# Optimization experiments

Hardware: AMD Instinct MI355X
Metric: run time of the kernel (lower is better)

## Reference

```python
import jax, jax.numpy as jnp
import numpy as np

B, T, N, F = 32, 4096, 11, 16
NUM_LABS = 20
H = 2 * F  # refine hidden dim
LN_EPS = 1e-5


def setup_inputs() -> dict:
    key = jax.random.key(0)
    ks = jax.random.split(key, 8)
    x = jax.random.normal(ks[0], (B, T, N, F), dtype=jnp.float32)
    lab_idx = jax.random.randint(ks[1], (B,), 0, NUM_LABS)
    # projection: identity + small noise, per lab
    projection = (jnp.eye(N, dtype=jnp.float32)[None].repeat(NUM_LABS, axis=0)
                  + 0.01 * jax.random.normal(ks[2], (NUM_LABS, N, N), dtype=jnp.float32))
    bias = jnp.zeros((NUM_LABS, 1, N, F), dtype=jnp.float32)
    w1 = jax.random.normal(ks[3], (F, H), dtype=jnp.float32) / np.sqrt(F)
    b1 = jnp.zeros((H,), dtype=jnp.float32)
    ln_g = jnp.ones((H,), dtype=jnp.float32)
    ln_b = jnp.zeros((H,), dtype=jnp.float32)
    w2 = jax.random.normal(ks[4], (H, F), dtype=jnp.float32) / np.sqrt(H)
    b2 = jnp.zeros((F,), dtype=jnp.float32)
    return {"x": x, "lab_idx": lab_idx, "projection": projection, "bias": bias,
            "w1": w1, "b1": b1, "ln_g": ln_g, "ln_b": ln_b, "w2": w2, "b2": b2}


def reference(x, lab_idx, projection, bias, w1, b1, ln_g, ln_b, w2, b2):
    # gather per-sample projection / bias by lab index
    W = projection[lab_idx]          # [b, n, n]
    Bb = bias[lab_idx]               # [b, 1, n, f]
    # torch: bmm(x^T, W) then transpose -> out[b,t,m,f] = sum_n x[b,t,n,f] * W[b,n,m]
    out = jnp.einsum('btnf,bnm->btmf', x, W) + Bb
    # refine MLP: Linear -> LayerNorm -> GELU(exact) -> Linear
    h = out @ w1 + b1                                    # [b,t,n,2f]
    mu = jnp.mean(h, axis=-1, keepdims=True)
    var = jnp.var(h, axis=-1, keepdims=True)
    h = (h - mu) / jnp.sqrt(var + LN_EPS) * ln_g + ln_b
    h = jax.nn.gelu(h, approximate=False)
    return h @ w2 + b2
```

## Files before the change

kernel.cpp:

```cpp
#include <hip/hip_runtime.h>
#include <hip/hip_bf16.h>
#include <math.h>

#define BB 32
#define TT 4096
#define NN 11
#define FF 16
#define HH 32
#define LN_EPS 1e-5f
#define TOTAL_ROWS (BB * TT * NN)
#define ROWS_PER_BLOCK 256
#define NBLOCKS (TOTAL_ROWS / ROWS_PER_BLOCK)
#define BLOCKS_PER_BATCH (TT * NN / ROWS_PER_BLOCK)

typedef __attribute__((ext_vector_type(8))) short short8;
typedef __attribute__((ext_vector_type(4))) float f32x4;

union Frag { unsigned u[4]; uint4 u4; short8 v; };

__device__ __forceinline__ unsigned pack2_bf16(float a, float b) {
    __hip_bfloat162 p = __float22bfloat162_rn(make_float2(a, b));
    union { __hip_bfloat162 h; unsigned u; } cvt; cvt.h = p; return cvt.u;
}
__device__ __forceinline__ unsigned short to_bf16u(float a) {
    __hip_bfloat16 h = __float2bfloat16(a);
    union { __hip_bfloat16 h; unsigned short u; } cvt; cvt.h = h; return cvt.u;
}

__device__ __forceinline__ float fast_gelu(float v) {
    const float v2 = v * v;
    const float c  = fmaf(0.044715f, v2, 1.0f);
    const float t  = v * c * 1.5957691216057308f;
    const float e  = __expf(-t);
    return v * __builtin_amdgcn_rcpf(1.0f + e);
}

__global__ __launch_bounds__(256) void fused_proj_mlp_mfma(
    const float* __restrict__ x,
    const int*   __restrict__ lab_idx,
    const float* __restrict__ proj,
    const float* __restrict__ bias,
    const float* __restrict__ w1,
    const float* __restrict__ b1,
    const float* __restrict__ ln_g,
    const float* __restrict__ ln_b,
    const float* __restrict__ w2,
    const float* __restrict__ b2,
    float*       __restrict__ out)
{
    __shared__ unsigned o_st[4][64][12];
    __shared__ unsigned short h_st[4][4][16][40];

    const int tid  = threadIdx.x;
    const int wv   = tid >> 6;
    const int lane = tid & 63;
    const int q    = lane >> 4;
    const int c    = lane & 15;

    const int row      = blockIdx.x * ROWS_PER_BLOCK + tid;
    const unsigned token = (unsigned)row / 11u;
    const int m        = row - (int)(token * 11u);
    const int bidx     = blockIdx.x / BLOCKS_PER_BATCH;
    const int lab      = lab_idx[bidx];

    Frag b1a, b1b, b2f;
    #pragma unroll
    for (int d = 0; d < 4; ++d) {
        const int k0 = 8 * q + 2 * d;
        float wa0 = 0.f, wa1 = 0.f, wb0 = 0.f, wb1 = 0.f;
        if (q < 2) {
            wa0 = w1[k0 * HH + c];        wa1 = w1[(k0 + 1) * HH + c];
            wb0 = w1[k0 * HH + 16 + c];   wb1 = w1[(k0 + 1) * HH + 16 + c];
        }
        b1a.u[d] = pack2_bf16(wa0, wa1);
        b1b.u[d] = pack2_bf16(wb0, wb1);
        b2f.u[d] = pack2_bf16(w2[k0 * FF + c], w2[(k0 + 1) * FF + c]);
    }
    const float b1c_a = b1[c], b1c_b = b1[16 + c], b2c = b2[c];

    float g8[8], e8[8];
    {
        const float4* gp = reinterpret_cast<const float4*>(ln_g + 8 * q);
        const float4* bp = reinterpret_cast<const float4*>(ln_b + 8 * q);
        float4 g0 = gp[0], g1 = gp[1], e0 = bp[0], e1 = bp[1];
        g8[0]=g0.x; g8[1]=g0.y; g8[2]=g0.z; g8[3]=g0.w;
        g8[4]=g1.x; g8[5]=g1.y; g8[6]=g1.z; g8[7]=g1.w;
        e8[0]=e0.x; e8[1]=e0.y; e8[2]=e0.z; e8[3]=e0.w;
        e8[4]=e1.x; e8[5]=e1.y; e8[6]=e1.z; e8[7]=e1.w;
    }

    const float4* xp4 = reinterpret_cast<const float4*>(x) + (size_t)token * (NN * FF / 4);
    const float*  Wp  = proj + (size_t)lab * (NN * NN) + m;
    const float4* bp4 = reinterpret_cast<const float4*>(bias) + (size_t)lab * (NN * FF / 4) + m * (FF / 4);

    float o[FF];
    #pragma unroll
    for (int f4 = 0; f4 < FF / 4; ++f4) {
        float4 v = bp4[f4];
        o[f4*4+0] = v.x; o[f4*4+1] = v.y; o[f4*4+2] = v.z; o[f4*4+3] = v.w;
    }
    #pragma unroll
    for (int n = 0; n < NN; ++n) {
        const float wnm = Wp[n * NN];
        #pragma unroll
        for (int f4 = 0; f4 < FF / 4; ++f4) {
            float4 v = xp4[n * (FF / 4) + f4];
            o[f4*4+0] = fmaf(v.x, wnm, o[f4*4+0]);
            o[f4*4+1] = fmaf(v.y, wnm, o[f4*4+1]);
            o[f4*4+2] = fmaf(v.z, wnm, o[f4*4+2]);
            o[f4*4+3] = fmaf(v.w, wnm, o[f4*4+3]);
        }
    }

    {
        unsigned op[8];
        #pragma unroll
        for (int d = 0; d < 8; ++d) op[d] = pack2_bf16(o[2*d], o[2*d+1]);
        uint4* dst = reinterpret_cast<uint4*>(&o_st[wv][lane][0]);
        dst[0] = make_uint4(op[0], op[1], op[2], op[3]);
        dst[1] = make_uint4(op[4], op[5], op[6], op[7]);
    }
    __syncthreads();

    const int qo = (q & 1) * 4;

    #pragma unroll
    for (int tt = 0; tt < 4; ++tt) {
        Frag a1;
        a1.u4 = *reinterpret_cast<const uint4*>(&o_st[wv][tt * 16 + c][qo]);
        f32x4 acc1a = { b1c_a, b1c_a, b1c_a, b1c_a };
        f32x4 acc1b = { b1c_b, b1c_b, b1c_b, b1c_b };
        acc1a = __builtin_amdgcn_mfma_f32_16x16x32_bf16(a1.v, b1a.v, acc1a, 0, 0, 0);
        acc1b = __builtin_amdgcn_mfma_f32_16x16x32_bf16(a1.v, b1b.v, acc1b, 0, 0, 0);

        #pragma unroll
        for (int i = 0; i < 4; ++i) {
            h_st[wv][tt][q * 4 + i][c]      = to_bf16u(acc1a[i]);
            h_st[wv][tt][q * 4 + i][16 + c] = to_bf16u(acc1b[i]);
        }
        __syncthreads();

        Frag a2r;
        a2r.u4 = *reinterpret_cast<const uint4*>(&h_st[wv][tt][c][8 * q]);
        float hv[8];
        #pragma unroll
        for (int d = 0; d < 4; ++d) {
            union { unsigned u; float f; } lo, hi;
            lo.u = a2r.u[d] << 16; hi.u = a2r.u[d] & 0xffff0000u;
            hv[2*d] = lo.f; hv[2*d+1] = hi.f;
        }

        float s = 0.f, ss = 0.f;
        #pragma unroll
        for (int d = 0; d < 8; ++d) { s += hv[d]; ss = fmaf(hv[d], hv[d], ss); }
        s  += __shfl_xor(s, 16);  s  += __shfl_xor(s, 32);
        ss += __shfl_xor(ss, 16); ss += __shfl_xor(ss, 32);
        const float mu   = s * (1.f / HH);
        const float var  = ss * (1.f / HH) - mu * mu;
        const float rstd = rsqrtf(var + LN_EPS);
        const float nb   = -mu * rstd;

        Frag a2;
        #pragma unroll
        for (int d = 0; d < 4; ++d) {
            float v0 = fmaf(fmaf(hv[2*d],   rstd, nb), g8[2*d],   e8[2*d]);
            float v1 = fmaf(fmaf(hv[2*d+1], rstd, nb), g8[2*d+1], e8[2*d+1]);
            a2.u[d] = pack2_bf16(fast_gelu(v0), fast_gelu(v1));
        }

        f32x4 acc2 = { b2c, b2c, b2c, b2c };
        acc2 = __builtin_amdgcn_mfma_f32_16x16x32_bf16(a2.v, b2f.v, acc2, 0, 0, 0);

        float* orow = out + ((size_t)(blockIdx.x * ROWS_PER_BLOCK + wv * 64 + tt * 16 + q * 4) * FF + c);
        #pragma unroll
        for (int i = 0; i < 4; ++i) orow[(size_t)i * FF] = acc2[i];
    }
}

extern "C" void kernel_launch(void* const* d_in, const int* in_sizes, int n_in,
                              void* d_out, int out_size, void* d_ws, size_t ws_size,
                              hipStream_t stream) {
    const float* x       = (const float*)d_in[0];
    const int*   lab_idx = (const int*)  d_in[1];
    const float* proj    = (const float*)d_in[2];
    const float* bias    = (const float*)d_in[3];
    const float* w1      = (const float*)d_in[4];
    const float* b1      = (const float*)d_in[5];
    const float* ln_g    = (const float*)d_in[6];
    const float* ln_b    = (const float*)d_in[7];
    const float* w2      = (const float*)d_in[8];
    const float* b2      = (const float*)d_in[9];
    float* out = (float*)d_out;

    fused_proj_mlp_mfma<<<NBLOCKS, 256, 0, stream>>>(
        x, lab_idx, proj, bias, w1, b1, ln_g, ln_b, w2, b2, out);
}
```

Before: 222.9 us.

## Transpose MFMA operands to keep hidden activations in registers

Swaps the MFMA operand roles so the weights become the A operand and the projected activations the B operand. Each lane then holds full hidden columns in its accumulators, so LayerNorm and GELU run directly on the fp32 MFMA results. This removes the bf16 round trip through the shared-memory h_st buffer and the block-wide __syncthreads inside the loop, and drops the barrier after the o_st write. The second matmul's input is rearranged with cross-lane shuffles instead, and outputs are written as float4 stores. The cost is extra shuffle instructions, and correctness now relies on each wave reading only its own o_st region without a barrier.

```diff
diff --git a/kernel.cpp b/kernel.cpp
--- a/kernel.cpp
+++ b/kernel.cpp
@@ -22,10 +22,6 @@
     __hip_bfloat162 p = __float22bfloat162_rn(make_float2(a, b));
     union { __hip_bfloat162 h; unsigned u; } cvt; cvt.h = p; return cvt.u;
 }
-__device__ __forceinline__ unsigned short to_bf16u(float a) {
-    __hip_bfloat16 h = __float2bfloat16(a);
-    union { __hip_bfloat16 h; unsigned short u; } cvt; cvt.h = h; return cvt.u;
-}
 
 __device__ __forceinline__ float fast_gelu(float v) {
     const float v2 = v * v;
@@ -35,7 +31,7 @@
     return v * __builtin_amdgcn_rcpf(1.0f + e);
 }
 
-__global__ __launch_bounds__(256) void fused_proj_mlp_mfma(
+__global__ __launch_bounds__(256) void fused_proj_mlp_t(
     const float* __restrict__ x,
     const int*   __restrict__ lab_idx,
     const float* __restrict__ proj,
@@ -49,7 +45,6 @@
     float*       __restrict__ out)
 {
     __shared__ unsigned o_st[4][64][12];
-    __shared__ unsigned short h_st[4][4][16][40];
 
     const int tid  = threadIdx.x;
     const int wv   = tid >> 6;
@@ -57,37 +52,37 @@
     const int q    = lane >> 4;
     const int c    = lane & 15;
 
-    const int row      = blockIdx.x * ROWS_PER_BLOCK + tid;
+    const int row        = blockIdx.x * ROWS_PER_BLOCK + tid;
     const unsigned token = (unsigned)row / 11u;
-    const int m        = row - (int)(token * 11u);
-    const int bidx     = blockIdx.x / BLOCKS_PER_BATCH;
-    const int lab      = lab_idx[bidx];
+    const int m          = row - (int)(token * 11u);
+    const int lab        = lab_idx[blockIdx.x / BLOCKS_PER_BATCH];
 
-    Frag b1a, b1b, b2f;
+    Frag a1c0, a1c1, a2f;
     #pragma unroll
     for (int d = 0; d < 4; ++d) {
         const int k0 = 8 * q + 2 * d;
         float wa0 = 0.f, wa1 = 0.f, wb0 = 0.f, wb1 = 0.f;
         if (q < 2) {
-            wa0 = w1[k0 * HH + c];        wa1 = w1[(k0 + 1) * HH + c];
-            wb0 = w1[k0 * HH + 16 + c];   wb1 = w1[(k0 + 1) * HH + 16 + c];
+            wa0 = w1[k0 * HH + c];       wa1 = w1[(k0 + 1) * HH + c];
+            wb0 = w1[k0 * HH + 16 + c];  wb1 = w1[(k0 + 1) * HH + 16 + c];
         }
-        b1a.u[d] = pack2_bf16(wa0, wa1);
-        b1b.u[d] = pack2_bf16(wb0, wb1);
-        b2f.u[d] = pack2_bf16(w2[k0 * FF + c], w2[(k0 + 1) * FF + c]);
+        a1c0.u[d] = pack2_bf16(wa0, wa1);
+        a1c1.u[d] = pack2_bf16(wb0, wb1);
+        a2f.u[d]  = pack2_bf16(w2[k0 * FF + c], w2[(k0 + 1) * FF + c]);
     }
-    const float b1c_a = b1[c], b1c_b = b1[16 + c], b2c = b2[c];
 
-    float g8[8], e8[8];
-    {
-        const float4* gp = reinterpret_cast<const float4*>(ln_g + 8 * q);
-        const float4* bp = reinterpret_cast<const float4*>(ln_b + 8 * q);
-        float4 g0 = gp[0], g1 = gp[1], e0 = bp[0], e1 = bp[1];
-        g8[0]=g0.x; g8[1]=g0.y; g8[2]=g0.z; g8[3]=g0.w;
-        g8[4]=g1.x; g8[5]=g1.y; g8[6]=g1.z; g8[7]=g1.w;
-        e8[0]=e0.x; e8[1]=e0.y; e8[2]=e0.z; e8[3]=e0.w;
-        e8[4]=e1.x; e8[5]=e1.y; e8[6]=e1.z; e8[7]=e1.w;
-    }
+    float4 b1v0 = *reinterpret_cast<const float4*>(b1 + 4 * q);
+    float4 b1v1 = *reinterpret_cast<const float4*>(b1 + 16 + 4 * q);
+    float4 b2v  = *reinterpret_cast<const float4*>(b2 + 4 * q);
+    float4 g0   = *reinterpret_cast<const float4*>(ln_g + 4 * q);
+    float4 g1   = *reinterpret_cast<const float4*>(ln_g + 16 + 4 * q);
+    float4 e0   = *reinterpret_cast<const float4*>(ln_b + 4 * q);
+    float4 e1   = *reinterpret_cast<const float4*>(ln_b + 16 + 4 * q);
+    float g0a[4] = {g0.x, g0.y, g0.z, g0.w}, g1a[4] = {g1.x, g1.y, g1.z, g1.w};
+    float e0a[4] = {e0.x, e0.y, e0.z, e0.w}, e1a[4] = {e1.x, e1.y, e1.z, e1.w};
+    float b1a0[4] = {b1v0.x, b1v0.y, b1v0.z, b1v0.w};
+    float b1a1[4] = {b1v1.x, b1v1.y, b1v1.z, b1v1.w};
+    float b2a[4]  = {b2v.x, b2v.y, b2v.z, b2v.w};
 
     const float4* xp4 = reinterpret_cast<const float4*>(x) + (size_t)token * (NN * FF / 4);
     const float*  Wp  = proj + (size_t)lab * (NN * NN) + m;
@@ -113,67 +108,71 @@
     }
 
     {
-        unsigned op[8];
+        unsigned p[8];
         #pragma unroll
-        for (int d = 0; d < 8; ++d) op[d] = pack2_bf16(o[2*d], o[2*d+1]);
+        for (int d = 0; d < 8; ++d) p[d] = pack2_bf16(o[2*d], o[2*d+1]);
         uint4* dst = reinterpret_cast<uint4*>(&o_st[wv][lane][0]);
-        dst[0] = make_uint4(op[0], op[1], op[2], op[3]);
-        dst[1] = make_uint4(op[4], op[5], op[6], op[7]);
+        dst[0] = make_uint4(p[0], p[1], p[2], p[3]);
+        dst[1] = make_uint4(p[4], p[5], p[6], p[7]);
     }
-    __syncthreads();
 
-    const int qo = (q & 1) * 4;
+    const int rowbase = blockIdx.x * ROWS_PER_BLOCK + wv * 64;
+    const int srcA = (q & 1) * 32 + c;
+    const int srcB = srcA + 16;
 
     #pragma unroll
     for (int tt = 0; tt < 4; ++tt) {
-        Frag a1;
-        a1.u4 = *reinterpret_cast<const uint4*>(&o_st[wv][tt * 16 + c][qo]);
-        f32x4 acc1a = { b1c_a, b1c_a, b1c_a, b1c_a };
-        f32x4 acc1b = { b1c_b, b1c_b, b1c_b, b1c_b };
-        acc1a = __builtin_amdgcn_mfma_f32_16x16x32_bf16(a1.v, b1a.v, acc1a, 0, 0, 0);
-        acc1b = __builtin_amdgcn_mfma_f32_16x16x32_bf16(a1.v, b1b.v, acc1b, 0, 0, 0);
+        Frag B1;
+        B1.u4 = *reinterpret_cast<const uint4*>(&o_st[wv][tt * 16 + c][(q & 1) * 4]);
 
-        #pragma unroll
-        for (int i = 0; i < 4; ++i) {
-            h_st[wv][tt][q * 4 + i][c]      = to_bf16u(acc1a[i]);
-            h_st[wv][tt][q * 4 + i][16 + c] = to_bf16u(acc1b[i]);
-        }
-        __syncthreads();
-
-        Frag a2r;
-        a2r.u4 = *reinterpret_cast<const uint4*>(&h_st[wv][tt][c][8 * q]);
-        float hv[8];
-        #pragma unroll
-        for (int d = 0; d < 4; ++d) {
-            union { unsigned u; float f; } lo, hi;
-            lo.u = a2r.u[d] << 16; hi.u = a2r.u[d] & 0xffff0000u;
-            hv[2*d] = lo.f; hv[2*d+1] = hi.f;
-        }
+        f32x4 accA = { b1a0[0], b1a0[1], b1a0[2], b1a0[3] };
+        f32x4 accB = { b1a1[0], b1a1[1], b1a1[2], b1a1[3] };
+        accA = __builtin_amdgcn_mfma_f32_16x16x32_bf16(a1c0.v, B1.v, accA, 0, 0, 0);
+        accB = __builtin_amdgcn_mfma_f32_16x16x32_bf16(a1c1.v, B1.v, accB, 0, 0, 0);
 
         float s = 0.f, ss = 0.f;
         #pragma unroll
-        for (int d = 0; d < 8; ++d) { s += hv[d]; ss = fmaf(hv[d], hv[d], ss); }
-        s  += __shfl_xor(s, 16);  s  += __shfl_xor(s, 32);
-        ss += __shfl_xor(ss, 16); ss += __shfl_xor(ss, 32);
+        for (int i = 0; i < 4; ++i) {
+            s += accA[i] + accB[i];
+            ss = fmaf(accA[i], accA[i], ss);
+            ss = fmaf(accB[i], accB[i], ss);
+        }
+        s  += __shfl_xor(s, 16, 64);  s  += __shfl_xor(s, 32, 64);
+        ss += __shfl_xor(ss, 16, 64); ss += __shfl_xor(ss, 32, 64);
         const float mu   = s * (1.f / HH);
         const float var  = ss * (1.f / HH) - mu * mu;
         const float rstd = rsqrtf(var + LN_EPS);
         const float nb   = -mu * rstd;
 
-        Frag a2;
+        float ga[4], gb[4];
         #pragma unroll
-        for (int d = 0; d < 4; ++d) {
-            float v0 = fmaf(fmaf(hv[2*d],   rstd, nb), g8[2*d],   e8[2*d]);
-            float v1 = fmaf(fmaf(hv[2*d+1], rstd, nb), g8[2*d+1], e8[2*d+1]);
-            a2.u[d] = pack2_bf16(fast_gelu(v0), fast_gelu(v1));
+        for (int i = 0; i < 4; ++i) {
+            ga[i] = fast_gelu(fmaf(fmaf(accA[i], rstd, nb), g0a[i], e0a[i]));
+            gb[i] = fast_gelu(fmaf(fmaf(accB[i], rstd, nb), g1a[i], e1a[i]));
+        }
+        const unsigned c0d0 = pack2_bf16(ga[0], ga[1]);
+        const unsigned c0d1 = pack2_bf16(ga[2], ga[3]);
+        const unsigned c1d0 = pack2_bf16(gb[0], gb[1]);
+        const unsigned c1d1 = pack2_bf16(gb[2], gb[3]);
+
+        Frag B2;
+        {
+            unsigned lo, hi;
+            lo = __shfl((int)c0d0, srcA, 64); hi = __shfl((int)c1d0, srcA, 64);
+            B2.u[0] = (q < 2) ? lo : hi;
+            lo = __shfl((int)c0d1, srcA, 64); hi = __shfl((int)c1d1, srcA, 64);
+            B2.u[1] = (q < 2) ? lo : hi;
+            lo = __shfl((int)c0d0, srcB, 64); hi = __shfl((int)c1d0, srcB, 64);
+            B2.u[2] = (q < 2) ? lo : hi;
+            lo = __shfl((int)c0d1, srcB, 64); hi = __shfl((int)c1d1, srcB, 64);
+            B2.u[3] = (q < 2) ? lo : hi;
         }
 
-        f32x4 acc2 = { b2c, b2c, b2c, b2c };
-        acc2 = __builtin_amdgcn_mfma_f32_16x16x32_bf16(a2.v, b2f.v, acc2, 0, 0, 0);
+        f32x4 acc2 = { b2a[0], b2a[1], b2a[2], b2a[3] };
+        acc2 = __builtin_amdgcn_mfma_f32_16x16x32_bf16(a2f.v, B2.v, acc2, 0, 0, 0);
 
-        float* orow = out + ((size_t)(blockIdx.x * ROWS_PER_BLOCK + wv * 64 + tt * 16 + q * 4) * FF + c);
-        #pragma unroll
-        for (int i = 0; i < 4; ++i) orow[(size_t)i * FF] = acc2[i];
+        float4* dst = reinterpret_cast<float4*>(out + (size_t)(rowbase + tt * 16 + c) * FF + 4 * q);
+        *dst = make_float4(acc2[0], acc2[1], acc2[2], acc2[3]);
     }
 }
 
@@ -192,6 +191,6 @@
     const float* b2      = (const float*)d_in[9];
     float* out = (float*)d_out;
 
-    fused_proj_mlp_mfma<<<NBLOCKS, 256, 0, stream>>>(
+    fused_proj_mlp_t<<<NBLOCKS, 256, 0, stream>>>(
         x, lab_idx, proj, bias, w1, b1, ln_g, ln_b, w2, b2, out);
 }
```

Result: slower. 231.6 us (+3.9%).
